# Performance work log

Measured on AMD Instinct MI355X. Metric: run time of the kernel, lower is better.

The kernel has to match this reference:

```python
import jax, jax.numpy as jnp
import numpy as np

TOL = 1e-4
MAX_ITER = 50
D = 512
B = 65536


def setup_inputs() -> dict:
    key = jax.random.key(0)
    kx, kw = jax.random.split(key)
    x = jax.random.normal(kx, (B, D), dtype=jnp.float32)
    # scale weight so the tanh fixed-point iteration is contractive
    W = jax.random.normal(kw, (D, D), dtype=jnp.float32) * (0.5 / np.sqrt(D))
    return {"x": x, "W": W}


def reference(x, W):
    """z_{k+1} = tanh(z_k @ W.T + x), starting from z_0 = 0, with
    early exit when ||z_k - z_{k+1}||_F < TOL (z frozen after convergence,
    equivalent to the torch `break`). Fixed-length scan keeps it jit-able
    and reverse-mode differentiable."""

    def step(carry, _):
        z, done = carry
        z_next = jnp.tanh(z @ W.T + x)            # [B, D]
        err = jnp.linalg.norm(z - z_next)         # Frobenius norm, scalar
        z = jnp.where(done, z, z_next)
        done = done | (err < TOL)
        return (z, done), None

    z0 = jnp.zeros_like(x)
    (z, _), _ = jax.lax.scan(step, (z0, jnp.array(False)), None, length=MAX_ITER)
    return z
```

## Files before the change

### kernel.cpp

```cpp
#include <hip/hip_runtime.h>
#include <hip/hip_fp16.h>


#define DDIM  512
#define MTILE 64
#define NITER 50

typedef _Float16 half8  __attribute__((ext_vector_type(8)));
typedef _Float16 half4v __attribute__((ext_vector_type(4)));
typedef float    float4v __attribute__((ext_vector_type(4)));

__device__ __forceinline__ float fast_tanh(float t) {
    float e = __builtin_amdgcn_exp2f(t * 2.8853900817779268f);
    return 1.0f - 2.0f * __builtin_amdgcn_rcpf(e + 1.0f);
}

__device__ __forceinline__ int zaddr(int m, int k) {
    return (((k >> 5) * 4 + (m >> 4)) << 9) + (((m & 15) + (((k >> 3) & 3) << 4)) << 3) + (k & 7);
}

__global__ void wpack_kernel(const float* __restrict__ W, _Float16* __restrict__ Wpk) {
    int gid  = blockIdx.x * blockDim.x + threadIdx.x;
    int ks   = gid >> 11;
    int nf   = (gid >> 6) & 31;
    int lane = gid & 63;
    int row  = nf * 16 + (lane & 15);
    int col  = ks * 32 + (lane >> 4) * 8;
    const float* src = W + row * DDIM + col;
    half8 h;
#pragma unroll
    for (int j = 0; j < 8; ++j) h[j] = (_Float16)src[j];
    *(half8*)(Wpk + (size_t)gid * 8) = h;
}

__global__ __launch_bounds__(512, 2)
void fixpoint_kernel(const float* __restrict__ x,
                     const _Float16* __restrict__ Wpk,
                     float* __restrict__ out) {
    __shared__ __align__(16) _Float16 zsh[2][MTILE * DDIM];

    const int tid  = threadIdx.x;
    const int lane = tid & 63;
    const int wid  = tid >> 6;
    const int l15  = lane & 15;
    const int quad = lane >> 4;
    const int nf0  = wid * 4;

    const int row_blk = blockIdx.x * MTILE;
    const half8* Wv = (const half8*)Wpk + nf0 * 64 + lane;

    half8 A0[4], A1[4], A2[4], A3[4];
#pragma unroll
    for (int f = 0; f < 4; ++f) A0[f] = Wv[f * 64];
#pragma unroll
    for (int f = 0; f < 4; ++f) A1[f] = Wv[2048 + f * 64];
#pragma unroll
    for (int f = 0; f < 4; ++f) A2[f] = Wv[4096 + f * 64];
#pragma unroll
    for (int f = 0; f < 4; ++f) A3[f] = Wv[6144 + f * 64];

    float4v xr[4][4];
#pragma unroll
    for (int f = 0; f < 4; ++f) {
        int n = (nf0 + f) * 16 + quad * 4;
#pragma unroll
        for (int mf = 0; mf < 4; ++mf) {
            const float4v* xp = (const float4v*)(x + (size_t)(row_blk + mf * 16 + l15) * DDIM + n);
            xr[f][mf] = __builtin_nontemporal_load(xp);
        }
    }

#pragma unroll
    for (int f = 0; f < 4; ++f) {
        int n = (nf0 + f) * 16 + quad * 4;
#pragma unroll
        for (int mf = 0; mf < 4; ++mf) {
            int m = mf * 16 + l15;
            half4v h;
#pragma unroll
            for (int j = 0; j < 4; ++j) h[j] = (_Float16)fast_tanh(xr[f][mf][j]);
            *(half4v*)(&zsh[0][zaddr(m, n)]) = h;
        }
    }
    __syncthreads();

    int p = 0;
    for (int it = 0; it < NITER - 1; ++it) {
        const _Float16* zr = &zsh[p][0];

        half8 B0[4], B1[4];
#pragma unroll
        for (int mf = 0; mf < 4; ++mf) B0[mf] = *(const half8*)(zr + (mf * 64 + lane) * 8);
#pragma unroll
        for (int mf = 0; mf < 4; ++mf) B1[mf] = *(const half8*)(zr + ((4 + mf) * 64 + lane) * 8);

        float4v acc[4][4];
#pragma unroll
        for (int f = 0; f < 4; ++f)
#pragma unroll
            for (int mf = 0; mf < 4; ++mf) acc[f][mf] = xr[f][mf];

#pragma unroll
        for (int ks = 0; ks < 16; ++ks) {
            half8* Ac = ((ks & 3) == 0) ? A0 : ((ks & 3) == 1) ? A1 : ((ks & 3) == 2) ? A2 : A3;
            half8* Bc = (ks & 1) ? B1 : B0;
#pragma unroll
            for (int f = 0; f < 4; ++f)
#pragma unroll
                for (int mf = 0; mf < 4; ++mf)
                    acc[f][mf] = __builtin_amdgcn_mfma_f32_16x16x32_f16(Ac[f], Bc[mf], acc[f][mf], 0, 0, 0);
            {
                int ka = (ks + 4) & 15;
#pragma unroll
                for (int f = 0; f < 4; ++f) Ac[f] = Wv[ka * 2048 + f * 64];
            }
            if (ks < 14) {
#pragma unroll
                for (int mf = 0; mf < 4; ++mf)
                    Bc[mf] = *(const half8*)(zr + (((ks + 2) * 4 + mf) * 64 + lane) * 8);
            }
        }

        if (it < NITER - 2) {
            _Float16* zw = &zsh[p ^ 1][0];
#pragma unroll
            for (int f = 0; f < 4; ++f) {
                int n = (nf0 + f) * 16 + quad * 4;
#pragma unroll
                for (int mf = 0; mf < 4; ++mf) {
                    int m = mf * 16 + l15;
                    half4v h;
#pragma unroll
                    for (int j = 0; j < 4; ++j) h[j] = (_Float16)fast_tanh(acc[f][mf][j]);
                    *(half4v*)(zw + zaddr(m, n)) = h;
                }
            }
            __syncthreads();
            p ^= 1;
        } else {
#pragma unroll
            for (int f = 0; f < 4; ++f) {
                int n = (nf0 + f) * 16 + quad * 4;
#pragma unroll
                for (int mf = 0; mf < 4; ++mf) {
                    float4v v;
#pragma unroll
                    for (int j = 0; j < 4; ++j) v[j] = fast_tanh(acc[f][mf][j]);
                    float4v* op = (float4v*)(out + (size_t)(row_blk + mf * 16 + l15) * DDIM + n);
                    __builtin_nontemporal_store(v, op);
                }
            }
        }
    }
}

extern "C" void kernel_launch(void* const* d_in, const int* in_sizes, int n_in,
                              void* d_out, int out_size, void* d_ws, size_t ws_size,
                              hipStream_t stream) {
    const float* x = (const float*)d_in[0];
    const float* W = (const float*)d_in[1];
    _Float16* Wpk = (_Float16*)d_ws;
    float* out = (float*)d_out;

    wpack_kernel<<<128, 256, 0, stream>>>(W, Wpk);
    fixpoint_kernel<<<65536 / MTILE, 512, 0, stream>>>(x, Wpk, out);
}
```

Before: 3.594 ms.

## Double waves per block and stream x from memory to cut register pressure

Blocks grow from 512 to 1024 threads, so each wave computes 2 output column fragments instead of 4. The W register prefetch ring shrinks from four to two stages. The x tile is no longer held in registers across iterations. It is reloaded from global memory in every iteration's epilogue and added before tanh. The aim is to lower VGPR use and double the resident waves per CU to better hide latency, at the cost of extra x traffic each iteration, a shorter W prefetch distance and more waves at each barrier.

```diff
diff --git a/kernel.cpp b/kernel.cpp
--- a/kernel.cpp
+++ b/kernel.cpp
@@ -33,7 +33,7 @@
     *(half8*)(Wpk + (size_t)gid * 8) = h;
 }
 
-__global__ __launch_bounds__(512, 2)
+__global__ __launch_bounds__(1024, 4)
 void fixpoint_kernel(const float* __restrict__ x,
                      const _Float16* __restrict__ Wpk,
                      float* __restrict__ out) {
@@ -44,45 +44,31 @@
     const int wid  = tid >> 6;
     const int l15  = lane & 15;
     const int quad = lane >> 4;
-    const int nf0  = wid * 4;
+    const int nf0  = wid * 2;
 
     const int row_blk = blockIdx.x * MTILE;
     const half8* Wv = (const half8*)Wpk + nf0 * 64 + lane;
 
-    half8 A0[4], A1[4], A2[4], A3[4];
 #pragma unroll
-    for (int f = 0; f < 4; ++f) A0[f] = Wv[f * 64];
-#pragma unroll
-    for (int f = 0; f < 4; ++f) A1[f] = Wv[2048 + f * 64];
-#pragma unroll
-    for (int f = 0; f < 4; ++f) A2[f] = Wv[4096 + f * 64];
-#pragma unroll
-    for (int f = 0; f < 4; ++f) A3[f] = Wv[6144 + f * 64];
-
-    float4v xr[4][4];
-#pragma unroll
-    for (int f = 0; f < 4; ++f) {
+    for (int f = 0; f < 2; ++f) {
         int n = (nf0 + f) * 16 + quad * 4;
 #pragma unroll
         for (int mf = 0; mf < 4; ++mf) {
             const float4v* xp = (const float4v*)(x + (size_t)(row_blk + mf * 16 + l15) * DDIM + n);
-            xr[f][mf] = __builtin_nontemporal_load(xp);
-        }
-    }
-
-#pragma unroll
-    for (int f = 0; f < 4; ++f) {
-        int n = (nf0 + f) * 16 + quad * 4;
-#pragma unroll
-        for (int mf = 0; mf < 4; ++mf) {
-            int m = mf * 16 + l15;
+            float4v xv = __builtin_nontemporal_load(xp);
             half4v h;
 #pragma unroll
-            for (int j = 0; j < 4; ++j) h[j] = (_Float16)fast_tanh(xr[f][mf][j]);
-            *(half4v*)(&zsh[0][zaddr(m, n)]) = h;
+            for (int j = 0; j < 4; ++j) h[j] = (_Float16)fast_tanh(xv[j]);
+            *(half4v*)(&zsh[0][zaddr(mf * 16 + l15, n)]) = h;
         }
     }
     __syncthreads();
+
+    half8 X0[2], X1[2];
+#pragma unroll
+    for (int f = 0; f < 2; ++f) X0[f] = Wv[f * 64];
+#pragma unroll
+    for (int f = 0; f < 2; ++f) X1[f] = Wv[(32 + f) * 64];
 
     int p = 0;
     for (int it = 0; it < NITER - 1; ++it) {
@@ -94,25 +80,25 @@
 #pragma unroll
         for (int mf = 0; mf < 4; ++mf) B1[mf] = *(const half8*)(zr + ((4 + mf) * 64 + lane) * 8);
 
-        float4v acc[4][4];
+        float4v acc[2][4];
 #pragma unroll
-        for (int f = 0; f < 4; ++f)
+        for (int f = 0; f < 2; ++f)
 #pragma unroll
-            for (int mf = 0; mf < 4; ++mf) acc[f][mf] = xr[f][mf];
+            for (int mf = 0; mf < 4; ++mf) acc[f][mf] = (float4v){0.f, 0.f, 0.f, 0.f};
 
 #pragma unroll
         for (int ks = 0; ks < 16; ++ks) {
-            half8* Ac = ((ks & 3) == 0) ? A0 : ((ks & 3) == 1) ? A1 : ((ks & 3) == 2) ? A2 : A3;
+            half8* Ac = (ks & 1) ? X1 : X0;
             half8* Bc = (ks & 1) ? B1 : B0;
 #pragma unroll
-            for (int f = 0; f < 4; ++f)
+            for (int f = 0; f < 2; ++f)
 #pragma unroll
                 for (int mf = 0; mf < 4; ++mf)
                     acc[f][mf] = __builtin_amdgcn_mfma_f32_16x16x32_f16(Ac[f], Bc[mf], acc[f][mf], 0, 0, 0);
             {
-                int ka = (ks + 4) & 15;
+                int ka = (ks + 2) & 15;
 #pragma unroll
-                for (int f = 0; f < 4; ++f) Ac[f] = Wv[ka * 2048 + f * 64];
+                for (int f = 0; f < 2; ++f) Ac[f] = Wv[(ka * 32 + f) * 64];
             }
             if (ks < 14) {
 #pragma unroll
@@ -124,28 +110,35 @@
         if (it < NITER - 2) {
             _Float16* zw = &zsh[p ^ 1][0];
 #pragma unroll
-            for (int f = 0; f < 4; ++f) {
+            for (int f = 0; f < 2; ++f) {
+                int n = (nf0 + f) * 16 + quad * 4;
+                float4v xv[4];
+#pragma unroll
+                for (int mf = 0; mf < 4; ++mf) {
+                    const float4v* xp = (const float4v*)(x + (size_t)(row_blk + mf * 16 + l15) * DDIM + n);
+                    xv[mf] = __builtin_nontemporal_load(xp);
+                }
+#pragma unroll
+                for (int mf = 0; mf < 4; ++mf) {
+                    half4v h;
+#pragma unroll
+                    for (int j = 0; j < 4; ++j) h[j] = (_Float16)fast_tanh(acc[f][mf][j] + xv[mf][j]);
+                    *(half4v*)(zw + zaddr(mf * 16 + l15, n)) = h;
+                }
+            }
+            asm volatile("s_waitcnt lgkmcnt(0)\n\ts_barrier" ::: "memory");
+            p ^= 1;
+        } else {
+#pragma unroll
+            for (int f = 0; f < 2; ++f) {
                 int n = (nf0 + f) * 16 + quad * 4;
 #pragma unroll
                 for (int mf = 0; mf < 4; ++mf) {
-                    int m = mf * 16 + l15;
-                    half4v h;
-#pragma unroll
-                    for (int j = 0; j < 4; ++j) h[j] = (_Float16)fast_tanh(acc[f][mf][j]);
-                    *(half4v*)(zw + zaddr(m, n)) = h;
-                }
-            }
-            __syncthreads();
-            p ^= 1;
-        } else {
-#pragma unroll
-            for (int f = 0; f < 4; ++f) {
-                int n = (nf0 + f) * 16 + quad * 4;
-#pragma unroll
-                for (int mf = 0; mf < 4; ++mf) {
+                    const float4v* xp = (const float4v*)(x + (size_t)(row_blk + mf * 16 + l15) * DDIM + n);
+                    float4v xv = __builtin_nontemporal_load(xp);
                     float4v v;
 #pragma unroll
-                    for (int j = 0; j < 4; ++j) v[j] = fast_tanh(acc[f][mf][j]);
+                    for (int j = 0; j < 4; ++j) v[j] = fast_tanh(acc[f][mf][j] + xv[j]);
                     float4v* op = (float4v*)(out + (size_t)(row_blk + mf * 16 + l15) * DDIM + n);
                     __builtin_nontemporal_store(v, op);
                 }
@@ -163,5 +156,5 @@
     float* out = (float*)d_out;
 
     wpack_kernel<<<128, 256, 0, stream>>>(W, Wpk);
-    fixpoint_kernel<<<65536 / MTILE, 512, 0, stream>>>(x, Wpk, out);
+    fixpoint_kernel<<<65536 / MTILE, 1024, 0, stream>>>(x, Wpk, out);
 }
```

Result: slower. 4.127 ms (+14.8%).

## Phase-lock blocks per XCD with atomic counters to share W fetches in L2

Applied to the files above, without the earlier changes.

Adds a soft cross-block barrier. Blocks on the same XCD are grouped into cohorts of 32 through atomic counters, and each iteration waits on a per-iteration counter so the cohort streams the same W slices at the same time and reuses them in L2. A spin limit falls back to free running so the grid cannot deadlock. It also cuts the W prefetch depth from four register stages to two, drops nontemporal loads for x, and adds a counter-init kernel. The risk is spin and atomic overhead, and the shallower W prefetch may expose global-load latency.

```diff
diff --git a/kernel.cpp b/kernel.cpp
--- a/kernel.cpp
+++ b/kernel.cpp
@@ -5,6 +5,12 @@
 #define DDIM  512
 #define MTILE 64
 #define NITER 50
+
+#define XCDS        8
+#define CUS_PER_XCD 32
+#define COH_MAX     8
+#define ITER_SLOTS  64
+#define MAXSPIN     400
 
 typedef _Float16 half8  __attribute__((ext_vector_type(8)));
 typedef _Float16 half4v __attribute__((ext_vector_type(4)));
@@ -17,6 +23,21 @@
 
 __device__ __forceinline__ int zaddr(int m, int k) {
     return (((k >> 5) * 4 + (m >> 4)) << 9) + (((m & 15) + (((k >> 3) & 3) << 4)) << 3) + (k & 7);
+}
+
+__device__ __forceinline__ void xcd_phase_lock(unsigned* c, bool& on) {
+    if (!on) return;
+    __hip_atomic_fetch_add(c, 1u, __ATOMIC_RELAXED, __HIP_MEMORY_SCOPE_AGENT);
+    int s = 0;
+    while (__hip_atomic_load(c, __ATOMIC_RELAXED, __HIP_MEMORY_SCOPE_AGENT) < CUS_PER_XCD) {
+        if (++s >= MAXSPIN) { on = false; return; }
+        __builtin_amdgcn_s_sleep(2);
+    }
+}
+
+__global__ void zinit_kernel(unsigned* __restrict__ ctr) {
+    int i = blockIdx.x * blockDim.x + threadIdx.x;
+    if (i < XCDS + XCDS * COH_MAX * ITER_SLOTS) ctr[i] = 0u;
 }
 
 __global__ void wpack_kernel(const float* __restrict__ W, _Float16* __restrict__ Wpk) {
@@ -36,7 +57,8 @@
 __global__ __launch_bounds__(512, 2)
 void fixpoint_kernel(const float* __restrict__ x,
                      const _Float16* __restrict__ Wpk,
-                     float* __restrict__ out) {
+                     float* __restrict__ out,
+                     unsigned* __restrict__ ctr) {
     __shared__ __align__(16) _Float16 zsh[2][MTILE * DDIM];
 
     const int tid  = threadIdx.x;
@@ -49,15 +71,16 @@
     const int row_blk = blockIdx.x * MTILE;
     const half8* Wv = (const half8*)Wpk + nf0 * 64 + lane;
 
-    half8 A0[4], A1[4], A2[4], A3[4];
-#pragma unroll
-    for (int f = 0; f < 4; ++f) A0[f] = Wv[f * 64];
-#pragma unroll
-    for (int f = 0; f < 4; ++f) A1[f] = Wv[2048 + f * 64];
-#pragma unroll
-    for (int f = 0; f < 4; ++f) A2[f] = Wv[4096 + f * 64];
-#pragma unroll
-    for (int f = 0; f < 4; ++f) A3[f] = Wv[6144 + f * 64];
+    bool lock_on = true;
+    unsigned lockbase = 0;
+    if (tid == 0) {
+        unsigned xcd;
+        asm volatile("s_getreg_b32 %0, hwreg(HW_REG_XCC_ID)" : "=s"(xcd));
+        xcd &= (XCDS - 1);
+        unsigned t = __hip_atomic_fetch_add(ctr + xcd, 1u, __ATOMIC_RELAXED,
+                                            __HIP_MEMORY_SCOPE_AGENT);
+        lockbase = XCDS + (xcd * COH_MAX + ((t >> 5) & (COH_MAX - 1))) * ITER_SLOTS;
+    }
 
     float4v xr[4][4];
 #pragma unroll
@@ -65,10 +88,15 @@
         int n = (nf0 + f) * 16 + quad * 4;
 #pragma unroll
         for (int mf = 0; mf < 4; ++mf) {
-            const float4v* xp = (const float4v*)(x + (size_t)(row_blk + mf * 16 + l15) * DDIM + n);
-            xr[f][mf] = __builtin_nontemporal_load(xp);
+            xr[f][mf] = *(const float4v*)(x + (size_t)(row_blk + mf * 16 + l15) * DDIM + n);
         }
     }
+
+    half8 A0[4], A1[4];
+#pragma unroll
+    for (int f = 0; f < 4; ++f) A0[f] = Wv[f * 64];
+#pragma unroll
+    for (int f = 0; f < 4; ++f) A1[f] = Wv[(32 + f) * 64];
 
 #pragma unroll
     for (int f = 0; f < 4; ++f) {
@@ -82,7 +110,8 @@
             *(half4v*)(&zsh[0][zaddr(m, n)]) = h;
         }
     }
-    __syncthreads();
+    if (tid == 0) xcd_phase_lock(ctr + lockbase + 0, lock_on);
+    asm volatile("s_waitcnt lgkmcnt(0)\n\ts_barrier" ::: "memory");
 
     int p = 0;
     for (int it = 0; it < NITER - 1; ++it) {
@@ -102,7 +131,7 @@
 
 #pragma unroll
         for (int ks = 0; ks < 16; ++ks) {
-            half8* Ac = ((ks & 3) == 0) ? A0 : ((ks & 3) == 1) ? A1 : ((ks & 3) == 2) ? A2 : A3;
+            half8* Ac = (ks & 1) ? A1 : A0;
             half8* Bc = (ks & 1) ? B1 : B0;
 #pragma unroll
             for (int f = 0; f < 4; ++f)
@@ -110,9 +139,9 @@
                 for (int mf = 0; mf < 4; ++mf)
                     acc[f][mf] = __builtin_amdgcn_mfma_f32_16x16x32_f16(Ac[f], Bc[mf], acc[f][mf], 0, 0, 0);
             {
-                int ka = (ks + 4) & 15;
+                int ka = (ks + 2) & 15;
 #pragma unroll
-                for (int f = 0; f < 4; ++f) Ac[f] = Wv[ka * 2048 + f * 64];
+                for (int f = 0; f < 4; ++f) Ac[f] = Wv[(ka * 32 + f) * 64];
             }
             if (ks < 14) {
 #pragma unroll
@@ -135,7 +164,8 @@
                     *(half4v*)(zw + zaddr(m, n)) = h;
                 }
             }
-            __syncthreads();
+            if (tid == 0) xcd_phase_lock(ctr + lockbase + (it + 1), lock_on);
+            asm volatile("s_waitcnt lgkmcnt(0)\n\ts_barrier" ::: "memory");
             p ^= 1;
         } else {
 #pragma unroll
@@ -160,8 +190,10 @@
     const float* x = (const float*)d_in[0];
     const float* W = (const float*)d_in[1];
     _Float16* Wpk = (_Float16*)d_ws;
+    unsigned* ctr = (unsigned*)((char*)d_ws + 512 * 1024);
     float* out = (float*)d_out;
 
+    zinit_kernel<<<17, 256, 0, stream>>>(ctr);
     wpack_kernel<<<128, 256, 0, stream>>>(W, Wpk);
-    fixpoint_kernel<<<65536 / MTILE, 512, 0, stream>>>(x, Wpk, out);
+    fixpoint_kernel<<<65536 / MTILE, 512, 0, stream>>>(x, Wpk, out, ctr);
 }
```

Result: faster. 3.484 ms (-3.1%).

## Stagger per-block K-slice order and shrink W prefetch depth

Applied to the files above, without the earlier changes.

Each block now starts its K loop at a phase derived from its block index, so concurrent blocks read different W slices from L2 instead of all hitting the same addresses at once. The W register prefetch depth drops from four slices to two, freeing registers but leaving less latency hiding for the global W loads. The x load becomes a plain load instead of nontemporal, and __syncthreads is replaced by an explicit lgkmcnt wait plus s_barrier, which skips waiting on outstanding vector-memory loads.

```diff
diff --git a/kernel.cpp b/kernel.cpp
--- a/kernel.cpp
+++ b/kernel.cpp
@@ -47,17 +47,18 @@
     const int nf0  = wid * 4;
 
     const int row_blk = blockIdx.x * MTILE;
+    const int phase = ((blockIdx.x >> 3) ^ ((blockIdx.x & 7) << 1)) & 15;
+
     const half8* Wv = (const half8*)Wpk + nf0 * 64 + lane;
 
-    half8 A0[4], A1[4], A2[4], A3[4];
+    half8 A0[4], A1[4];
+    {
+        int k0 = phase, k1 = (phase + 1) & 15;
 #pragma unroll
-    for (int f = 0; f < 4; ++f) A0[f] = Wv[f * 64];
+        for (int f = 0; f < 4; ++f) A0[f] = Wv[(k0 * 32 + f) * 64];
 #pragma unroll
-    for (int f = 0; f < 4; ++f) A1[f] = Wv[2048 + f * 64];
-#pragma unroll
-    for (int f = 0; f < 4; ++f) A2[f] = Wv[4096 + f * 64];
-#pragma unroll
-    for (int f = 0; f < 4; ++f) A3[f] = Wv[6144 + f * 64];
+        for (int f = 0; f < 4; ++f) A1[f] = Wv[(k1 * 32 + f) * 64];
+    }
 
     float4v xr[4][4];
 #pragma unroll
@@ -65,8 +66,7 @@
         int n = (nf0 + f) * 16 + quad * 4;
 #pragma unroll
         for (int mf = 0; mf < 4; ++mf) {
-            const float4v* xp = (const float4v*)(x + (size_t)(row_blk + mf * 16 + l15) * DDIM + n);
-            xr[f][mf] = __builtin_nontemporal_load(xp);
+            xr[f][mf] = *(const float4v*)(x + (size_t)(row_blk + mf * 16 + l15) * DDIM + n);
         }
     }
 
@@ -82,17 +82,20 @@
             *(half4v*)(&zsh[0][zaddr(m, n)]) = h;
         }
     }
-    __syncthreads();
+    asm volatile("s_waitcnt lgkmcnt(0)\n\ts_barrier" ::: "memory");
 
     int p = 0;
     for (int it = 0; it < NITER - 1; ++it) {
         const _Float16* zr = &zsh[p][0];
 
         half8 B0[4], B1[4];
+        {
+            int k0 = phase, k1 = (phase + 1) & 15;
 #pragma unroll
-        for (int mf = 0; mf < 4; ++mf) B0[mf] = *(const half8*)(zr + (mf * 64 + lane) * 8);
+            for (int mf = 0; mf < 4; ++mf) B0[mf] = *(const half8*)(zr + ((k0 * 4 + mf) * 64 + lane) * 8);
 #pragma unroll
-        for (int mf = 0; mf < 4; ++mf) B1[mf] = *(const half8*)(zr + ((4 + mf) * 64 + lane) * 8);
+            for (int mf = 0; mf < 4; ++mf) B1[mf] = *(const half8*)(zr + ((k1 * 4 + mf) * 64 + lane) * 8);
+        }
 
         float4v acc[4][4];
 #pragma unroll
@@ -102,22 +105,20 @@
 
 #pragma unroll
         for (int ks = 0; ks < 16; ++ks) {
-            half8* Ac = ((ks & 3) == 0) ? A0 : ((ks & 3) == 1) ? A1 : ((ks & 3) == 2) ? A2 : A3;
+            half8* Ac = (ks & 1) ? A1 : A0;
             half8* Bc = (ks & 1) ? B1 : B0;
 #pragma unroll
             for (int f = 0; f < 4; ++f)
 #pragma unroll
                 for (int mf = 0; mf < 4; ++mf)
                     acc[f][mf] = __builtin_amdgcn_mfma_f32_16x16x32_f16(Ac[f], Bc[mf], acc[f][mf], 0, 0, 0);
-            {
-                int ka = (ks + 4) & 15;
+            int ka = (phase + ks + 2) & 15;
 #pragma unroll
-                for (int f = 0; f < 4; ++f) Ac[f] = Wv[ka * 2048 + f * 64];
-            }
+            for (int f = 0; f < 4; ++f) Ac[f] = Wv[(ka * 32 + f) * 64];
             if (ks < 14) {
 #pragma unroll
                 for (int mf = 0; mf < 4; ++mf)
-                    Bc[mf] = *(const half8*)(zr + (((ks + 2) * 4 + mf) * 64 + lane) * 8);
+                    Bc[mf] = *(const half8*)(zr + ((ka * 4 + mf) * 64 + lane) * 8);
             }
         }
 
@@ -135,7 +136,7 @@
                     *(half4v*)(zw + zaddr(m, n)) = h;
                 }
             }
-            __syncthreads();
+            asm volatile("s_waitcnt lgkmcnt(0)\n\ts_barrier" ::: "memory");
             p ^= 1;
         } else {
 #pragma unroll
```

Result: faster. 3.249 ms (-9.6%).
